# Optimization experiments

Hardware: AMD Instinct MI355X
Metric: run time of the kernel (lower is better)

The kernel has to match this reference:

```python
import jax, jax.numpy as jnp
import numpy as np

B, NW, D, K = 16384, 32, 64, 512  # batch, n_windows, embedding_dim, codebook_size


def setup_inputs() -> dict:
    key = jax.random.key(0)
    k1, k2 = jax.random.split(key)
    ze = jax.random.normal(k1, (B, NW * D), dtype=jnp.float32)
    codebook = jax.random.normal(k2, (K, D), dtype=jnp.float32)
    return {"ze": ze, "codebook": codebook}


def reference(ze, codebook):
    # window-based VQ: split last dim into NW windows of size D, quantize each
    zew = ze.reshape(B, NW, D)
    # squared distances: ||ze||^2 + ||e||^2 - 2 ze.e^T  -> [B, NW, K]
    sq_norm = (
        jnp.sum(zew * zew, axis=-1, keepdims=True)
        + jnp.sum(codebook * codebook, axis=-1)
        - 2.0 * jnp.einsum("bwd,kd->bwk", zew, codebook)
    )
    indices = jnp.argmin(sq_norm, axis=-1)  # [B, NW]
    zq = codebook[indices].reshape(ze.shape)  # gather + concat over windows

    vq_e_loss = jnp.mean((zq - jax.lax.stop_gradient(ze)) ** 2)
    vq_commit_loss = jnp.mean((jax.lax.stop_gradient(zq) - ze) ** 2)

    # entropy term: counts of each code usage divided by 10 (as in original)
    counts = jnp.bincount(indices.reshape(-1), length=K)
    probs = counts.astype(jnp.float32) / 10.0
    entropy = jnp.sum(probs * jnp.log(probs + 1e-10))
    return indices, zq, vq_e_loss, vq_commit_loss, entropy
```

## Files before the change

kernel.cpp:

```cpp
#include <hip/hip_runtime.h>
#include <math.h>

#define DIM 64
#define KCB 512
#define NWIN 524288
#define ZQN (NWIN * DIM)
#define WPT 512
#define TPB 2
#define NBLK (NWIN / (WPT * TPB))

typedef __attribute__((ext_vector_type(8))) short bf16x8;
typedef __attribute__((ext_vector_type(4))) float f32x4;

__device__ __forceinline__ unsigned bfbits(float f) { return __float_as_uint(f) >> 16; }

__device__ __forceinline__ int4 pack8(float4 a, float4 b) {
    int4 r;
    r.x = (int)(bfbits(a.x) | (__float_as_uint(a.y) & 0xffff0000u));
    r.y = (int)(bfbits(a.z) | (__float_as_uint(a.w) & 0xffff0000u));
    r.z = (int)(bfbits(b.x) | (__float_as_uint(b.y) & 0xffff0000u));
    r.w = (int)(bfbits(b.z) | (__float_as_uint(b.w) & 0xffff0000u));
    return r;
}

__global__ __launch_bounds__(512, 4) void vq_fused_kernel(
    const float* __restrict__ ze, const float* __restrict__ cb,
    float* __restrict__ out_idx, float* __restrict__ zq,
    int* __restrict__ counts, float* __restrict__ lossAcc)
{
    __shared__ int4  bfr[4096];
    __shared__ float norm_s[KCB];
    __shared__ int   idx_s[WPT];
    __shared__ int   hist_s[KCB];
    __shared__ float lpart[8];

    const int t    = threadIdx.x;
    const int lane = t & 63;
    const int wv   = t >> 6;
    const int q    = lane >> 4;
    const int l15  = lane & 15;
    const long blk = blockIdx.x;

    hist_s[t] = 0;

    {
        const float4* c4 = (const float4*)cb;
        float s = 0.f;
#pragma unroll
        for (int i = 0; i < 16; ++i) {
            float4 v = c4[t * 16 + i];
            s += v.x * v.x + v.y * v.y + v.z * v.z + v.w * v.w;
        }
        norm_s[t] = 0.5f * s;
    }

#pragma unroll
    for (int i = 0; i < 8; ++i) {
        int f = i * 512 + t;
        int L = f & 63, rest = f >> 6, h = rest & 1, c = rest >> 1;
        int n = c * 16 + (L & 15);
        int k = h * 32 + (L >> 4) * 8;
        const float4* s4 = (const float4*)(cb + n * DIM + k);
        bfr[(c * 2 + h) * 64 + L] = pack8(s4[0], s4[1]);
    }

    const float4* z4b = (const float4*)ze;
    float4*       zq4 = (float4*)zq;
    float lsum = 0.f;

    float4 abuf[16];
    {
        const float4* z4 = z4b + blk * TPB * WPT * 16;
        const int m = wv * 64 + l15;
#pragma unroll
        for (int tt = 0; tt < 4; ++tt)
#pragma unroll
            for (int h = 0; h < 2; ++h)
#pragma unroll
                for (int i = 0; i < 2; ++i)
                    abuf[tt * 4 + h * 2 + i] = z4[(m + tt * 16) * 16 + h * 8 + q * 2 + i];
    }
    __syncthreads();

#pragma unroll
    for (int tl = 0; tl < TPB; ++tl) {
        const long g = blk * TPB + tl;

        bf16x8 afrag[4][2];
        float  znorm[4];
#pragma unroll
        for (int tt = 0; tt < 4; ++tt) {
            float part = 0.f;
#pragma unroll
            for (int h = 0; h < 2; ++h) {
                float4 a0 = abuf[tt * 4 + h * 2], a1 = abuf[tt * 4 + h * 2 + 1];
                part += a0.x*a0.x + a0.y*a0.y + a0.z*a0.z + a0.w*a0.w
                      + a1.x*a1.x + a1.y*a1.y + a1.z*a1.z + a1.w*a1.w;
                int4 p = pack8(a0, a1);
                p.x ^= 0x80008000; p.y ^= 0x80008000;
                p.z ^= 0x80008000; p.w ^= 0x80008000;
                afrag[tt][h] = __builtin_bit_cast(bf16x8, p);
            }
            part += __shfl_xor(part, 16, 64);
            part += __shfl_xor(part, 32, 64);
            znorm[tt] = part;
        }

        float best[4][4];
#pragma unroll
        for (int tt = 0; tt < 4; ++tt)
#pragma unroll
            for (int r = 0; r < 4; ++r) best[tt][r] = __uint_as_float(0x7e000000u);

        for (int cp = 0; cp < 16; ++cp) {
            f32x4 e0[4], e1[4];
            {
                const int c = 2 * cp;
                bf16x8 b0 = __builtin_bit_cast(bf16x8, bfr[(c * 2 + 0) * 64 + lane]);
                bf16x8 b1 = __builtin_bit_cast(bf16x8, bfr[(c * 2 + 1) * 64 + lane]);
                float nh = norm_s[c * 16 + l15];
                f32x4 nrm4 = {nh, nh, nh, nh};
#pragma unroll
                for (int tt = 0; tt < 4; ++tt) {
                    e0[tt] = __builtin_amdgcn_mfma_f32_16x16x32_bf16(afrag[tt][0], b0, nrm4, 0, 0, 0);
                    e0[tt] = __builtin_amdgcn_mfma_f32_16x16x32_bf16(afrag[tt][1], b1, e0[tt], 0, 0, 0);
                }
            }
            {
                const int c = 2 * cp + 1;
                bf16x8 b0 = __builtin_bit_cast(bf16x8, bfr[(c * 2 + 0) * 64 + lane]);
                bf16x8 b1 = __builtin_bit_cast(bf16x8, bfr[(c * 2 + 1) * 64 + lane]);
                float nh = norm_s[c * 16 + l15];
                f32x4 nrm4 = {nh, nh, nh, nh};
#pragma unroll
                for (int tt = 0; tt < 4; ++tt) {
                    e1[tt] = __builtin_amdgcn_mfma_f32_16x16x32_bf16(afrag[tt][0], b0, nrm4, 0, 0, 0);
                    e1[tt] = __builtin_amdgcn_mfma_f32_16x16x32_bf16(afrag[tt][1], b1, e1[tt], 0, 0, 0);
                }
            }
            const unsigned n0 = (unsigned)(2 * cp) * 16 + (unsigned)l15;
            const unsigned n1 = n0 + 16;
#pragma unroll
            for (int tt = 0; tt < 4; ++tt)
#pragma unroll
                for (int r = 0; r < 4; ++r) {
                    float p0 = __uint_as_float((__float_as_uint(e0[tt][r]) & ~511u) | n0);
                    float p1 = __uint_as_float((__float_as_uint(e1[tt][r]) & ~511u) | n1);
                    best[tt][r] = fminf(fminf(best[tt][r], p0), p1);
                }
        }

#pragma unroll
        for (int tt = 0; tt < 4; ++tt)
#pragma unroll
            for (int r = 0; r < 4; ++r) {
                float v = best[tt][r];
                v = fminf(v, __shfl_xor(v, 1, 64));
                v = fminf(v, __shfl_xor(v, 2, 64));
                v = fminf(v, __shfl_xor(v, 4, 64));
                v = fminf(v, __shfl_xor(v, 8, 64));
                best[tt][r] = v;
            }

        {
            int  r_act = l15 - q * 4;
            bool act   = (r_act >= 0) && (r_act < 4);
#pragma unroll
            for (int tt = 0; tt < 4; ++tt) {
                if (act) {
                    unsigned bb = __float_as_uint(best[tt][r_act]);
                    int   n  = (int)(bb & 511u);
                    float sc = __uint_as_float(bb & ~511u);
                    lsum += fmaf(2.f, sc, znorm[tt]);
                    idx_s[wv * 64 + tt * 16 + l15] = n;
                }
            }
        }

        if (tl < TPB - 1) {
            const float4* z4 = z4b + (g + 1) * WPT * 16;
            const int m = wv * 64 + l15;
#pragma unroll
            for (int tt = 0; tt < 4; ++tt)
#pragma unroll
                for (int h = 0; h < 2; ++h)
#pragma unroll
                    for (int i = 0; i < 2; ++i)
                        abuf[tt * 4 + h * 2 + i] = z4[(m + tt * 16) * 16 + h * 8 + q * 2 + i];
        }
        __syncthreads();

        out_idx[g * WPT + t] = (float)idx_s[t];
        atomicAdd(&hist_s[idx_s[t]], 1);

        {
            const long zb = g * WPT * 16;
#pragma unroll
            for (int it = 0; it < 16; ++it) {
                int w_loc = it * 32 + (t >> 4);
                int j  = t & 15;
                int n  = idx_s[w_loc];
                int c  = n >> 4, ln = n & 15;
                int h  = j >> 3;
                int q2 = (j >> 1) & 3;
                int4 v = bfr[(c * 2 + h) * 64 + q2 * 16 + ln];
                int a  = (j & 1) ? v.z : v.x;
                int b  = (j & 1) ? v.w : v.y;
                float4 o;
                o.x = __uint_as_float((unsigned)a << 16);
                o.y = __uint_as_float((unsigned)a & 0xffff0000u);
                o.z = __uint_as_float((unsigned)b << 16);
                o.w = __uint_as_float((unsigned)b & 0xffff0000u);
                zq4[zb + (long)w_loc * 16 + j] = o;
            }
        }
        __syncthreads();
    }

#pragma unroll
    for (int off = 32; off; off >>= 1) lsum += __shfl_down(lsum, off, 64);
    if (lane == 0) lpart[wv] = lsum;
    __syncthreads();
    if (t == 0) {
        float s = 0.f;
#pragma unroll
        for (int i = 0; i < 8; ++i) s += lpart[i];
        atomicAdd(lossAcc, s);
    }
    int h0 = hist_s[t];
    if (h0) atomicAdd(&counts[t], h0);
}

__global__ __launch_bounds__(512) void vq_finalize_kernel(
    const int* __restrict__ counts, const float* __restrict__ lossAcc,
    float* __restrict__ outs)
{
    __shared__ float partial[8];
    const int t = threadIdx.x;

    float p = (float)counts[t] * 0.1f;
    float term = p * logf(p + 1e-10f);
#pragma unroll
    for (int off = 32; off; off >>= 1) term += __shfl_down(term, off, 64);
    if ((t & 63) == 0) partial[t >> 6] = term;
    __syncthreads();
    if (t == 0) {
        float e = 0.f;
#pragma unroll
        for (int i = 0; i < 8; ++i) e += partial[i];
        float loss = lossAcc[0] / (float)ZQN;
        outs[0] = loss;
        outs[1] = loss;
        outs[2] = e;
    }
}

extern "C" void kernel_launch(void* const* d_in, const int* in_sizes, int n_in,
                              void* d_out, int out_size, void* d_ws, size_t ws_size,
                              hipStream_t stream) {
    const float* ze = (const float*)d_in[0];
    const float* cb = (const float*)d_in[1];
    float* out = (float*)d_out;

    float* out_idx = out;
    float* out_zq  = out + NWIN;
    float* out_scl = out + NWIN + (long)ZQN;

    int*   counts  = (int*)d_ws;
    float* lossAcc = (float*)((char*)d_ws + KCB * sizeof(int));
    hipMemsetAsync(d_ws, 0, KCB * sizeof(int) + sizeof(float), stream);

    vq_fused_kernel<<<NBLK, 512, 0, stream>>>(ze, cb, out_idx, out_zq, counts, lossAcc);
    vq_finalize_kernel<<<1, KCB, 0, stream>>>(counts, lossAcc, out_scl);
}
```

Before: 275.6 us.

## Use 1024-thread blocks with fewer tiles per wave and global-fp32 zq gather

```diff
diff --git a/kernel.cpp b/kernel.cpp
--- a/kernel.cpp
+++ b/kernel.cpp
@@ -7,6 +7,7 @@
 #define ZQN (NWIN * DIM)
 #define WPT 512
 #define TPB 2
+#define THREADS 1024
 #define NBLK (NWIN / (WPT * TPB))
 
 typedef __attribute__((ext_vector_type(8))) short bf16x8;
@@ -23,16 +24,16 @@
     return r;
 }
 
-__global__ __launch_bounds__(512, 4) void vq_fused_kernel(
+__global__ __launch_bounds__(THREADS, 8) void vq_fused_kernel(
     const float* __restrict__ ze, const float* __restrict__ cb,
     float* __restrict__ out_idx, float* __restrict__ zq,
     int* __restrict__ counts, float* __restrict__ lossAcc)
 {
     __shared__ int4  bfr[4096];
     __shared__ float norm_s[KCB];
-    __shared__ int   idx_s[WPT];
+    __shared__ int   idx_s[TPB][WPT];
     __shared__ int   hist_s[KCB];
-    __shared__ float lpart[8];
+    __shared__ float lpart[16];
 
     const int t    = threadIdx.x;
     const int lane = t & 63;
@@ -41,9 +42,8 @@
     const int l15  = lane & 15;
     const long blk = blockIdx.x;
 
-    hist_s[t] = 0;
-
-    {
+    if (t < KCB) {
+        hist_s[t] = 0;
         const float4* c4 = (const float4*)cb;
         float s = 0.f;
 #pragma unroll
@@ -55,8 +55,8 @@
     }
 
 #pragma unroll
-    for (int i = 0; i < 8; ++i) {
-        int f = i * 512 + t;
+    for (int i = 0; i < 4; ++i) {
+        int f = i * THREADS + t;
         int L = f & 63, rest = f >> 6, h = rest & 1, c = rest >> 1;
         int n = c * 16 + (L & 15);
         int k = h * 32 + (L >> 4) * 8;
@@ -65,35 +65,27 @@
     }
 
     const float4* z4b = (const float4*)ze;
+    const float4* c4g = (const float4*)cb;
     float4*       zq4 = (float4*)zq;
     float lsum = 0.f;
 
-    float4 abuf[16];
-    {
-        const float4* z4 = z4b + blk * TPB * WPT * 16;
-        const int m = wv * 64 + l15;
-#pragma unroll
-        for (int tt = 0; tt < 4; ++tt)
-#pragma unroll
-            for (int h = 0; h < 2; ++h)
-#pragma unroll
-                for (int i = 0; i < 2; ++i)
-                    abuf[tt * 4 + h * 2 + i] = z4[(m + tt * 16) * 16 + h * 8 + q * 2 + i];
-    }
     __syncthreads();
 
 #pragma unroll
     for (int tl = 0; tl < TPB; ++tl) {
         const long g = blk * TPB + tl;
-
-        bf16x8 afrag[4][2];
-        float  znorm[4];
-#pragma unroll
-        for (int tt = 0; tt < 4; ++tt) {
+        const float4* z4 = z4b + g * (long)(WPT * 16);
+        const int m = wv * 32 + l15;
+
+        bf16x8 afrag[2][2];
+        float  znorm[2];
+#pragma unroll
+        for (int tt = 0; tt < 2; ++tt) {
             float part = 0.f;
 #pragma unroll
             for (int h = 0; h < 2; ++h) {
-                float4 a0 = abuf[tt * 4 + h * 2], a1 = abuf[tt * 4 + h * 2 + 1];
+                float4 a0 = z4[(m + tt * 16) * 16 + h * 8 + q * 2 + 0];
+                float4 a1 = z4[(m + tt * 16) * 16 + h * 8 + q * 2 + 1];
                 part += a0.x*a0.x + a0.y*a0.y + a0.z*a0.z + a0.w*a0.w
                       + a1.x*a1.x + a1.y*a1.y + a1.z*a1.z + a1.w*a1.w;
                 int4 p = pack8(a0, a1);
@@ -106,14 +98,14 @@
             znorm[tt] = part;
         }
 
-        float best[4][4];
-#pragma unroll
-        for (int tt = 0; tt < 4; ++tt)
+        float best[2][4];
+#pragma unroll
+        for (int tt = 0; tt < 2; ++tt)
 #pragma unroll
             for (int r = 0; r < 4; ++r) best[tt][r] = __uint_as_float(0x7e000000u);
 
         for (int cp = 0; cp < 16; ++cp) {
-            f32x4 e0[4], e1[4];
+            f32x4 e0[2], e1[2];
             {
                 const int c = 2 * cp;
                 bf16x8 b0 = __builtin_bit_cast(bf16x8, bfr[(c * 2 + 0) * 64 + lane]);
@@ -121,7 +113,7 @@
                 float nh = norm_s[c * 16 + l15];
                 f32x4 nrm4 = {nh, nh, nh, nh};
 #pragma unroll
-                for (int tt = 0; tt < 4; ++tt) {
+                for (int tt = 0; tt < 2; ++tt) {
                     e0[tt] = __builtin_amdgcn_mfma_f32_16x16x32_bf16(afrag[tt][0], b0, nrm4, 0, 0, 0);
                     e0[tt] = __builtin_amdgcn_mfma_f32_16x16x32_bf16(afrag[tt][1], b1, e0[tt], 0, 0, 0);
                 }
@@ -133,7 +125,7 @@
                 float nh = norm_s[c * 16 + l15];
                 f32x4 nrm4 = {nh, nh, nh, nh};
 #pragma unroll
-                for (int tt = 0; tt < 4; ++tt) {
+                for (int tt = 0; tt < 2; ++tt) {
                     e1[tt] = __builtin_amdgcn_mfma_f32_16x16x32_bf16(afrag[tt][0], b0, nrm4, 0, 0, 0);
                     e1[tt] = __builtin_amdgcn_mfma_f32_16x16x32_bf16(afrag[tt][1], b1, e1[tt], 0, 0, 0);
                 }
@@ -141,7 +133,7 @@
             const unsigned n0 = (unsigned)(2 * cp) * 16 + (unsigned)l15;
             const unsigned n1 = n0 + 16;
 #pragma unroll
-            for (int tt = 0; tt < 4; ++tt)
+            for (int tt = 0; tt < 2; ++tt)
 #pragma unroll
                 for (int r = 0; r < 4; ++r) {
                     float p0 = __uint_as_float((__float_as_uint(e0[tt][r]) & ~511u) | n0);
@@ -151,7 +143,7 @@
         }
 
 #pragma unroll
-        for (int tt = 0; tt < 4; ++tt)
+        for (int tt = 0; tt < 2; ++tt)
 #pragma unroll
             for (int r = 0; r < 4; ++r) {
                 float v = best[tt][r];
@@ -162,59 +154,39 @@
                 best[tt][r] = v;
             }
 
-        {
-            int  r_act = l15 - q * 4;
-            bool act   = (r_act >= 0) && (r_act < 4);
-#pragma unroll
-            for (int tt = 0; tt < 4; ++tt) {
-                if (act) {
-                    unsigned bb = __float_as_uint(best[tt][r_act]);
+#pragma unroll
+        for (int r = 0; r < 4; ++r) {
+            if (l15 == q * 4 + r) {
+#pragma unroll
+                for (int tt = 0; tt < 2; ++tt) {
+                    unsigned bb = __float_as_uint(best[tt][r]);
                     int   n  = (int)(bb & 511u);
                     float sc = __uint_as_float(bb & ~511u);
                     lsum += fmaf(2.f, sc, znorm[tt]);
-                    idx_s[wv * 64 + tt * 16 + l15] = n;
-                }
-            }
-        }
-
-        if (tl < TPB - 1) {
-            const float4* z4 = z4b + (g + 1) * WPT * 16;
-            const int m = wv * 64 + l15;
-#pragma unroll
-            for (int tt = 0; tt < 4; ++tt)
-#pragma unroll
-                for (int h = 0; h < 2; ++h)
-#pragma unroll
-                    for (int i = 0; i < 2; ++i)
-                        abuf[tt * 4 + h * 2 + i] = z4[(m + tt * 16) * 16 + h * 8 + q * 2 + i];
-        }
+                    idx_s[tl][wv * 32 + tt * 16 + l15] = n;
+                }
+            }
+        }
+
         __syncthreads();
 
-        out_idx[g * WPT + t] = (float)idx_s[t];
-        atomicAdd(&hist_s[idx_s[t]], 1);
+        if (t < WPT) {
+            int n = idx_s[tl][t];
+            out_idx[g * WPT + t] = (float)n;
+            atomicAdd(&hist_s[n], 1);
+        }
 
         {
-            const long zb = g * WPT * 16;
-#pragma unroll
-            for (int it = 0; it < 16; ++it) {
-                int w_loc = it * 32 + (t >> 4);
+            const long zb = g * (long)(WPT * 16);
+#pragma unroll
+            for (int it = 0; it < 8; ++it) {
+                int w_loc = it * 64 + (t >> 4);
                 int j  = t & 15;
-                int n  = idx_s[w_loc];
-                int c  = n >> 4, ln = n & 15;
-                int h  = j >> 3;
-                int q2 = (j >> 1) & 3;
-                int4 v = bfr[(c * 2 + h) * 64 + q2 * 16 + ln];
-                int a  = (j & 1) ? v.z : v.x;
-                int b  = (j & 1) ? v.w : v.y;
-                float4 o;
-                o.x = __uint_as_float((unsigned)a << 16);
-                o.y = __uint_as_float((unsigned)a & 0xffff0000u);
-                o.z = __uint_as_float((unsigned)b << 16);
-                o.w = __uint_as_float((unsigned)b & 0xffff0000u);
-                zq4[zb + (long)w_loc * 16 + j] = o;
-            }
-        }
-        __syncthreads();
+                int n  = idx_s[tl][w_loc];
+                f32x4 o = *(const f32x4*)(c4g + n * 16 + j);
+                __builtin_nontemporal_store(o, (f32x4*)(zq4 + zb + (long)w_loc * 16 + j));
+            }
+        }
     }
 
 #pragma unroll
@@ -224,11 +196,13 @@
     if (t == 0) {
         float s = 0.f;
 #pragma unroll
-        for (int i = 0; i < 8; ++i) s += lpart[i];
+        for (int i = 0; i < 16; ++i) s += lpart[i];
         atomicAdd(lossAcc, s);
     }
-    int h0 = hist_s[t];
-    if (h0) atomicAdd(&counts[t], h0);
+    if (t < KCB) {
+        int h0 = hist_s[t];
+        if (h0) atomicAdd(&counts[t], h0);
+    }
 }
 
 __global__ __launch_bounds__(512) void vq_finalize_kernel(
@@ -270,6 +244,6 @@
     float* lossAcc = (float*)((char*)d_ws + KCB * sizeof(int));
     hipMemsetAsync(d_ws, 0, KCB * sizeof(int) + sizeof(float), stream);
 
-    vq_fused_kernel<<<NBLK, 512, 0, stream>>>(ze, cb, out_idx, out_zq, counts, lossAcc);
+    vq_fused_kernel<<<NBLK, THREADS, 0, stream>>>(ze, cb, out_idx, out_zq, counts, lossAcc);
     vq_finalize_kernel<<<1, KCB, 0, stream>>>(counts, lossAcc, out_scl);
 }
```

Result: slower. 307.0 us (+11.4%).

## Split zq gather into separate kernel and prefetch next tile earlier

Applied to the files above, without the earlier changes.

```diff
diff --git a/kernel.cpp b/kernel.cpp
--- a/kernel.cpp
+++ b/kernel.cpp
@@ -23,14 +23,13 @@
     return r;
 }
 
-__global__ __launch_bounds__(512, 4) void vq_fused_kernel(
+__global__ __launch_bounds__(512, 4) void vq_argmin_kernel(
     const float* __restrict__ ze, const float* __restrict__ cb,
-    float* __restrict__ out_idx, float* __restrict__ zq,
+    float* __restrict__ out_idx,
     int* __restrict__ counts, float* __restrict__ lossAcc)
 {
     __shared__ int4  bfr[4096];
     __shared__ float norm_s[KCB];
-    __shared__ int   idx_s[WPT];
     __shared__ int   hist_s[KCB];
     __shared__ float lpart[8];
 
@@ -40,6 +39,21 @@
     const int q    = lane >> 4;
     const int l15  = lane & 15;
     const long blk = blockIdx.x;
+
+    const float4* z4b = (const float4*)ze;
+
+    float4 abuf[16];
+    {
+        const float4* z4 = z4b + blk * (long)(TPB * WPT * 16);
+        const int m = wv * 64 + l15;
+#pragma unroll
+        for (int tt = 0; tt < 4; ++tt)
+#pragma unroll
+            for (int h = 0; h < 2; ++h)
+#pragma unroll
+                for (int i = 0; i < 2; ++i)
+                    abuf[tt * 4 + h * 2 + i] = z4[(m + tt * 16) * 16 + h * 8 + q * 2 + i];
+    }
 
     hist_s[t] = 0;
 
@@ -64,22 +78,7 @@
         bfr[(c * 2 + h) * 64 + L] = pack8(s4[0], s4[1]);
     }
 
-    const float4* z4b = (const float4*)ze;
-    float4*       zq4 = (float4*)zq;
     float lsum = 0.f;
-
-    float4 abuf[16];
-    {
-        const float4* z4 = z4b + blk * TPB * WPT * 16;
-        const int m = wv * 64 + l15;
-#pragma unroll
-        for (int tt = 0; tt < 4; ++tt)
-#pragma unroll
-            for (int h = 0; h < 2; ++h)
-#pragma unroll
-                for (int i = 0; i < 2; ++i)
-                    abuf[tt * 4 + h * 2 + i] = z4[(m + tt * 16) * 16 + h * 8 + q * 2 + i];
-    }
     __syncthreads();
 
 #pragma unroll
@@ -106,6 +105,18 @@
             znorm[tt] = part;
         }
 
+        if (tl < TPB - 1) {
+            const float4* z4 = z4b + (g + 1) * (long)(WPT * 16);
+            const int m = wv * 64 + l15;
+#pragma unroll
+            for (int tt = 0; tt < 4; ++tt)
+#pragma unroll
+                for (int h = 0; h < 2; ++h)
+#pragma unroll
+                    for (int i = 0; i < 2; ++i)
+                        abuf[tt * 4 + h * 2 + i] = z4[(m + tt * 16) * 16 + h * 8 + q * 2 + i];
+        }
+
         float best[4][4];
 #pragma unroll
         for (int tt = 0; tt < 4; ++tt)
@@ -162,59 +173,20 @@
                 best[tt][r] = v;
             }
 
-        {
-            int  r_act = l15 - q * 4;
-            bool act   = (r_act >= 0) && (r_act < 4);
-#pragma unroll
-            for (int tt = 0; tt < 4; ++tt) {
-                if (act) {
-                    unsigned bb = __float_as_uint(best[tt][r_act]);
+#pragma unroll
+        for (int r = 0; r < 4; ++r) {
+            if (l15 == q * 4 + r) {
+#pragma unroll
+                for (int tt = 0; tt < 4; ++tt) {
+                    unsigned bb = __float_as_uint(best[tt][r]);
                     int   n  = (int)(bb & 511u);
                     float sc = __uint_as_float(bb & ~511u);
                     lsum += fmaf(2.f, sc, znorm[tt]);
-                    idx_s[wv * 64 + tt * 16 + l15] = n;
-                }
-            }
-        }
-
-        if (tl < TPB - 1) {
-            const float4* z4 = z4b + (g + 1) * WPT * 16;
-            const int m = wv * 64 + l15;
-#pragma unroll
-            for (int tt = 0; tt < 4; ++tt)
-#pragma unroll
-                for (int h = 0; h < 2; ++h)
-#pragma unroll
-                    for (int i = 0; i < 2; ++i)
-                        abuf[tt * 4 + h * 2 + i] = z4[(m + tt * 16) * 16 + h * 8 + q * 2 + i];
-        }
-        __syncthreads();
-
-        out_idx[g * WPT + t] = (float)idx_s[t];
-        atomicAdd(&hist_s[idx_s[t]], 1);
-
-        {
-            const long zb = g * WPT * 16;
-#pragma unroll
-            for (int it = 0; it < 16; ++it) {
-                int w_loc = it * 32 + (t >> 4);
-                int j  = t & 15;
-                int n  = idx_s[w_loc];
-                int c  = n >> 4, ln = n & 15;
-                int h  = j >> 3;
-                int q2 = (j >> 1) & 3;
-                int4 v = bfr[(c * 2 + h) * 64 + q2 * 16 + ln];
-                int a  = (j & 1) ? v.z : v.x;
-                int b  = (j & 1) ? v.w : v.y;
-                float4 o;
-                o.x = __uint_as_float((unsigned)a << 16);
-                o.y = __uint_as_float((unsigned)a & 0xffff0000u);
-                o.z = __uint_as_float((unsigned)b << 16);
-                o.w = __uint_as_float((unsigned)b & 0xffff0000u);
-                zq4[zb + (long)w_loc * 16 + j] = o;
-            }
-        }
-        __syncthreads();
+                    out_idx[g * WPT + wv * 64 + tt * 16 + l15] = (float)n;
+                    atomicAdd(&hist_s[n], 1);
+                }
+            }
+        }
     }
 
 #pragma unroll
@@ -229,6 +201,27 @@
     }
     int h0 = hist_s[t];
     if (h0) atomicAdd(&counts[t], h0);
+}
+
+#define GELEMS (ZQN / 4)
+#define K2BLK 2048
+#define K2THR 256
+
+__global__ __launch_bounds__(K2THR) void vq_gather_kernel(
+    const float* __restrict__ idxf, const float* __restrict__ cb,
+    float* __restrict__ zq)
+{
+    const f32x4* c4 = (const f32x4*)cb;
+    f32x4*       z4 = (f32x4*)zq;
+    long i = (long)blockIdx.x * K2THR + threadIdx.x;
+    const long stride = (long)K2BLK * K2THR;
+#pragma unroll 4
+    for (; i < GELEMS; i += stride) {
+        long w = i >> 4;
+        int  j = (int)(i & 15);
+        int  n = (int)idxf[w];
+        z4[i] = c4[n * 16 + j];
+    }
 }
 
 __global__ __launch_bounds__(512) void vq_finalize_kernel(
@@ -270,6 +263,7 @@
     float* lossAcc = (float*)((char*)d_ws + KCB * sizeof(int));
     hipMemsetAsync(d_ws, 0, KCB * sizeof(int) + sizeof(float), stream);
 
-    vq_fused_kernel<<<NBLK, 512, 0, stream>>>(ze, cb, out_idx, out_zq, counts, lossAcc);
+    vq_argmin_kernel<<<NBLK, 512, 0, stream>>>(ze, cb, out_idx, counts, lossAcc);
+    vq_gather_kernel<<<K2BLK, K2THR, 0, stream>>>(out_idx, cb, out_zq);
     vq_finalize_kernel<<<1, KCB, 0, stream>>>(counts, lossAcc, out_scl);
 }
```

Result: slower. 304.0 us (+10.3%).

## Process one tile per block and issue ze loads before codebook setup

Applied to the files above, without the earlier changes.

```diff
diff --git a/kernel.cpp b/kernel.cpp
--- a/kernel.cpp
+++ b/kernel.cpp
@@ -6,8 +6,7 @@
 #define NWIN 524288
 #define ZQN (NWIN * DIM)
 #define WPT 512
-#define TPB 2
-#define NBLK (NWIN / (WPT * TPB))
+#define NBLK (NWIN / WPT)
 
 typedef __attribute__((ext_vector_type(8))) short bf16x8;
 typedef __attribute__((ext_vector_type(4))) float f32x4;
@@ -30,8 +29,8 @@
 {
     __shared__ int4  bfr[4096];
     __shared__ float norm_s[KCB];
+    __shared__ int   hist_s[KCB];
     __shared__ int   idx_s[WPT];
-    __shared__ int   hist_s[KCB];
     __shared__ float lpart[8];
 
     const int t    = threadIdx.x;
@@ -40,6 +39,21 @@
     const int q    = lane >> 4;
     const int l15  = lane & 15;
     const long blk = blockIdx.x;
+
+    const float4* z4b = (const float4*)ze;
+
+    float4 ld[16];
+    {
+        const float4* z4 = z4b + blk * (long)(WPT * 16);
+        const int m = wv * 64 + l15;
+#pragma unroll
+        for (int tt = 0; tt < 4; ++tt)
+#pragma unroll
+            for (int h = 0; h < 2; ++h)
+#pragma unroll
+                for (int i = 0; i < 2; ++i)
+                    ld[tt * 4 + h * 2 + i] = z4[(m + tt * 16) * 16 + h * 8 + q * 2 + i];
+    }
 
     hist_s[t] = 0;
 
@@ -64,157 +78,125 @@
         bfr[(c * 2 + h) * 64 + L] = pack8(s4[0], s4[1]);
     }
 
-    const float4* z4b = (const float4*)ze;
-    float4*       zq4 = (float4*)zq;
+    __syncthreads();
+
+    bf16x8 afrag[4][2];
+    float  znorm[4];
+#pragma unroll
+    for (int tt = 0; tt < 4; ++tt) {
+        float part = 0.f;
+#pragma unroll
+        for (int h = 0; h < 2; ++h) {
+            float4 a0 = ld[tt * 4 + h * 2], a1 = ld[tt * 4 + h * 2 + 1];
+            part += a0.x*a0.x + a0.y*a0.y + a0.z*a0.z + a0.w*a0.w
+                  + a1.x*a1.x + a1.y*a1.y + a1.z*a1.z + a1.w*a1.w;
+            int4 p = pack8(a0, a1);
+            p.x ^= 0x80008000; p.y ^= 0x80008000;
+            p.z ^= 0x80008000; p.w ^= 0x80008000;
+            afrag[tt][h] = __builtin_bit_cast(bf16x8, p);
+        }
+        part += __shfl_xor(part, 16, 64);
+        part += __shfl_xor(part, 32, 64);
+        znorm[tt] = part;
+    }
+
+    float best[4][4];
+#pragma unroll
+    for (int tt = 0; tt < 4; ++tt)
+#pragma unroll
+        for (int r = 0; r < 4; ++r) best[tt][r] = __uint_as_float(0x7e000000u);
+
+    for (int cp = 0; cp < 16; ++cp) {
+        f32x4 e0[4], e1[4];
+        {
+            const int c = 2 * cp;
+            bf16x8 b0 = __builtin_bit_cast(bf16x8, bfr[(c * 2 + 0) * 64 + lane]);
+            bf16x8 b1 = __builtin_bit_cast(bf16x8, bfr[(c * 2 + 1) * 64 + lane]);
+            float nh = norm_s[c * 16 + l15];
+            f32x4 nrm4 = {nh, nh, nh, nh};
+#pragma unroll
+            for (int tt = 0; tt < 4; ++tt) {
+                e0[tt] = __builtin_amdgcn_mfma_f32_16x16x32_bf16(afrag[tt][0], b0, nrm4, 0, 0, 0);
+                e0[tt] = __builtin_amdgcn_mfma_f32_16x16x32_bf16(afrag[tt][1], b1, e0[tt], 0, 0, 0);
+            }
+        }
+        {
+            const int c = 2 * cp + 1;
+            bf16x8 b0 = __builtin_bit_cast(bf16x8, bfr[(c * 2 + 0) * 64 + lane]);
+            bf16x8 b1 = __builtin_bit_cast(bf16x8, bfr[(c * 2 + 1) * 64 + lane]);
+            float nh = norm_s[c * 16 + l15];
+            f32x4 nrm4 = {nh, nh, nh, nh};
+#pragma unroll
+            for (int tt = 0; tt < 4; ++tt) {
+                e1[tt] = __builtin_amdgcn_mfma_f32_16x16x32_bf16(afrag[tt][0], b0, nrm4, 0, 0, 0);
+                e1[tt] = __builtin_amdgcn_mfma_f32_16x16x32_bf16(afrag[tt][1], b1, e1[tt], 0, 0, 0);
+            }
+        }
+        const unsigned n0 = (unsigned)(2 * cp) * 16 + (unsigned)l15;
+        const unsigned n1 = n0 + 16;
+#pragma unroll
+        for (int tt = 0; tt < 4; ++tt)
+#pragma unroll
+            for (int r = 0; r < 4; ++r) {
+                float p0 = __uint_as_float((__float_as_uint(e0[tt][r]) & ~511u) | n0);
+                float p1 = __uint_as_float((__float_as_uint(e1[tt][r]) & ~511u) | n1);
+                best[tt][r] = fminf(fminf(best[tt][r], p0), p1);
+            }
+    }
+
+#pragma unroll
+    for (int tt = 0; tt < 4; ++tt)
+#pragma unroll
+        for (int r = 0; r < 4; ++r) {
+            float v = best[tt][r];
+            v = fminf(v, __shfl_xor(v, 1, 64));
+            v = fminf(v, __shfl_xor(v, 2, 64));
+            v = fminf(v, __shfl_xor(v, 4, 64));
+            v = fminf(v, __shfl_xor(v, 8, 64));
+            best[tt][r] = v;
+        }
+
     float lsum = 0.f;
-
-    float4 abuf[16];
-    {
-        const float4* z4 = z4b + blk * TPB * WPT * 16;
-        const int m = wv * 64 + l15;
-#pragma unroll
-        for (int tt = 0; tt < 4; ++tt)
-#pragma unroll
-            for (int h = 0; h < 2; ++h)
-#pragma unroll
-                for (int i = 0; i < 2; ++i)
-                    abuf[tt * 4 + h * 2 + i] = z4[(m + tt * 16) * 16 + h * 8 + q * 2 + i];
-    }
-    __syncthreads();
-
-#pragma unroll
-    for (int tl = 0; tl < TPB; ++tl) {
-        const long g = blk * TPB + tl;
-
-        bf16x8 afrag[4][2];
-        float  znorm[4];
-#pragma unroll
-        for (int tt = 0; tt < 4; ++tt) {
-            float part = 0.f;
-#pragma unroll
-            for (int h = 0; h < 2; ++h) {
-                float4 a0 = abuf[tt * 4 + h * 2], a1 = abuf[tt * 4 + h * 2 + 1];
-                part += a0.x*a0.x + a0.y*a0.y + a0.z*a0.z + a0.w*a0.w
-                      + a1.x*a1.x + a1.y*a1.y + a1.z*a1.z + a1.w*a1.w;
-                int4 p = pack8(a0, a1);
-                p.x ^= 0x80008000; p.y ^= 0x80008000;
-                p.z ^= 0x80008000; p.w ^= 0x80008000;
-                afrag[tt][h] = __builtin_bit_cast(bf16x8, p);
-            }
-            part += __shfl_xor(part, 16, 64);
-            part += __shfl_xor(part, 32, 64);
-            znorm[tt] = part;
-        }
-
-        float best[4][4];
-#pragma unroll
-        for (int tt = 0; tt < 4; ++tt)
-#pragma unroll
-            for (int r = 0; r < 4; ++r) best[tt][r] = __uint_as_float(0x7e000000u);
-
-        for (int cp = 0; cp < 16; ++cp) {
-            f32x4 e0[4], e1[4];
-            {
-                const int c = 2 * cp;
-                bf16x8 b0 = __builtin_bit_cast(bf16x8, bfr[(c * 2 + 0) * 64 + lane]);
-                bf16x8 b1 = __builtin_bit_cast(bf16x8, bfr[(c * 2 + 1) * 64 + lane]);
-                float nh = norm_s[c * 16 + l15];
-                f32x4 nrm4 = {nh, nh, nh, nh};
-#pragma unroll
-                for (int tt = 0; tt < 4; ++tt) {
-                    e0[tt] = __builtin_amdgcn_mfma_f32_16x16x32_bf16(afrag[tt][0], b0, nrm4, 0, 0, 0);
-                    e0[tt] = __builtin_amdgcn_mfma_f32_16x16x32_bf16(afrag[tt][1], b1, e0[tt], 0, 0, 0);
-                }
-            }
-            {
-                const int c = 2 * cp + 1;
-                bf16x8 b0 = __builtin_bit_cast(bf16x8, bfr[(c * 2 + 0) * 64 + lane]);
-                bf16x8 b1 = __builtin_bit_cast(bf16x8, bfr[(c * 2 + 1) * 64 + lane]);
-                float nh = norm_s[c * 16 + l15];
-                f32x4 nrm4 = {nh, nh, nh, nh};
-#pragma unroll
-                for (int tt = 0; tt < 4; ++tt) {
-                    e1[tt] = __builtin_amdgcn_mfma_f32_16x16x32_bf16(afrag[tt][0], b0, nrm4, 0, 0, 0);
-                    e1[tt] = __builtin_amdgcn_mfma_f32_16x16x32_bf16(afrag[tt][1], b1, e1[tt], 0, 0, 0);
-                }
-            }
-            const unsigned n0 = (unsigned)(2 * cp) * 16 + (unsigned)l15;
-            const unsigned n1 = n0 + 16;
-#pragma unroll
-            for (int tt = 0; tt < 4; ++tt)
-#pragma unroll
-                for (int r = 0; r < 4; ++r) {
-                    float p0 = __uint_as_float((__float_as_uint(e0[tt][r]) & ~511u) | n0);
-                    float p1 = __uint_as_float((__float_as_uint(e1[tt][r]) & ~511u) | n1);
-                    best[tt][r] = fminf(fminf(best[tt][r], p0), p1);
-                }
-        }
-
-#pragma unroll
-        for (int tt = 0; tt < 4; ++tt)
-#pragma unroll
-            for (int r = 0; r < 4; ++r) {
-                float v = best[tt][r];
-                v = fminf(v, __shfl_xor(v, 1, 64));
-                v = fminf(v, __shfl_xor(v, 2, 64));
-                v = fminf(v, __shfl_xor(v, 4, 64));
-                v = fminf(v, __shfl_xor(v, 8, 64));
-                best[tt][r] = v;
-            }
-
-        {
-            int  r_act = l15 - q * 4;
-            bool act   = (r_act >= 0) && (r_act < 4);
+#pragma unroll
+    for (int r = 0; r < 4; ++r) {
+        if (l15 == q * 4 + r) {
 #pragma unroll
             for (int tt = 0; tt < 4; ++tt) {
-                if (act) {
-                    unsigned bb = __float_as_uint(best[tt][r_act]);
-                    int   n  = (int)(bb & 511u);
-                    float sc = __uint_as_float(bb & ~511u);
-                    lsum += fmaf(2.f, sc, znorm[tt]);
-                    idx_s[wv * 64 + tt * 16 + l15] = n;
-                }
-            }
-        }
-
-        if (tl < TPB - 1) {
-            const float4* z4 = z4b + (g + 1) * WPT * 16;
-            const int m = wv * 64 + l15;
-#pragma unroll
-            for (int tt = 0; tt < 4; ++tt)
-#pragma unroll
-                for (int h = 0; h < 2; ++h)
-#pragma unroll
-                    for (int i = 0; i < 2; ++i)
-                        abuf[tt * 4 + h * 2 + i] = z4[(m + tt * 16) * 16 + h * 8 + q * 2 + i];
-        }
-        __syncthreads();
-
-        out_idx[g * WPT + t] = (float)idx_s[t];
-        atomicAdd(&hist_s[idx_s[t]], 1);
-
-        {
-            const long zb = g * WPT * 16;
-#pragma unroll
-            for (int it = 0; it < 16; ++it) {
-                int w_loc = it * 32 + (t >> 4);
-                int j  = t & 15;
-                int n  = idx_s[w_loc];
-                int c  = n >> 4, ln = n & 15;
-                int h  = j >> 3;
-                int q2 = (j >> 1) & 3;
-                int4 v = bfr[(c * 2 + h) * 64 + q2 * 16 + ln];
-                int a  = (j & 1) ? v.z : v.x;
-                int b  = (j & 1) ? v.w : v.y;
-                float4 o;
-                o.x = __uint_as_float((unsigned)a << 16);
-                o.y = __uint_as_float((unsigned)a & 0xffff0000u);
-                o.z = __uint_as_float((unsigned)b << 16);
-                o.w = __uint_as_float((unsigned)b & 0xffff0000u);
-                zq4[zb + (long)w_loc * 16 + j] = o;
-            }
-        }
-        __syncthreads();
+                unsigned bb = __float_as_uint(best[tt][r]);
+                int   n  = (int)(bb & 511u);
+                float sc = __uint_as_float(bb & ~511u);
+                lsum += fmaf(2.f, sc, znorm[tt]);
+                idx_s[wv * 64 + tt * 16 + l15] = n;
+                atomicAdd(&hist_s[n], 1);
+            }
+        }
+    }
+
+    __syncthreads();
+
+    out_idx[blk * (long)WPT + t] = (float)idx_s[t];
+
+    {
+        float4* zq4 = (float4*)zq;
+        const long zb = blk * (long)(WPT * 16);
+#pragma unroll
+        for (int it = 0; it < 16; ++it) {
+            int w_loc = it * 32 + (t >> 4);
+            int j  = t & 15;
+            int n  = idx_s[w_loc];
+            int c  = n >> 4, ln = n & 15;
+            int h  = j >> 3;
+            int q2 = (j >> 1) & 3;
+            int4 v = bfr[(c * 2 + h) * 64 + q2 * 16 + ln];
+            int a  = (j & 1) ? v.z : v.x;
+            int b  = (j & 1) ? v.w : v.y;
+            float4 o;
+            o.x = __uint_as_float((unsigned)a << 16);
+            o.y = __uint_as_float((unsigned)a & 0xffff0000u);
+            o.z = __uint_as_float((unsigned)b << 16);
+            o.w = __uint_as_float((unsigned)b & 0xffff0000u);
+            zq4[zb + (long)w_loc * 16 + j] = o;
+        }
     }
 
 #pragma unroll
@@ -227,8 +209,10 @@
         for (int i = 0; i < 8; ++i) s += lpart[i];
         atomicAdd(lossAcc, s);
     }
-    int h0 = hist_s[t];
-    if (h0) atomicAdd(&counts[t], h0);
+    {
+        int h0 = hist_s[t];
+        if (h0) atomicAdd(&counts[t], h0);
+    }
 }
 
 __global__ __launch_bounds__(512) void vq_finalize_kernel(
```

After: 269.5 us. -2.2%, faster.
